# Kernel optimization log

Hardware: AMD Instinct MI355X
Metric: run time of the kernel (lower is better)

The kernel has to match this reference:

```python
import jax, jax.numpy as jnp
import numpy as np

N = 100000   # nodes
E = 1600000  # directed edges (avg degree 16)
IN, HID, OUT = 32, 64, 32


def setup_inputs() -> dict:
    key = jax.random.key(0)
    k0, k1, k2, k3 = jax.random.split(key, 4)
    x = jax.random.normal(k0, (N, IN), dtype=jnp.float32)
    edge_index = jax.random.randint(k1, (2, E), 0, N, dtype=jnp.int32)
    W1 = jax.random.normal(k2, (IN, HID), dtype=jnp.float32) * (1.0 / np.sqrt(IN))
    b1 = jnp.zeros((HID,), dtype=jnp.float32)
    W2 = jax.random.normal(k3, (HID, OUT), dtype=jnp.float32) * (1.0 / np.sqrt(HID))
    b2 = jnp.zeros((OUT,), dtype=jnp.float32)
    return {"x": x, "edge_index": edge_index, "W1": W1, "b1": b1, "W2": W2, "b2": b2}


def gcn_conv(x, src, dst, W, b, n):
    # GCNConv: D^{-1/2} (A + I) D^{-1/2} X W + b, deg computed after self-loops
    h = x @ W                                   # [N, d_out]
    ones = jnp.ones_like(dst, dtype=h.dtype)
    deg = jax.ops.segment_sum(ones, dst, num_segments=n)   # >= 1 (self-loops)
    dinv = jax.lax.rsqrt(jnp.maximum(deg, 1.0))
    norm = dinv[src] * dinv[dst]                # [E + N]
    agg = jax.ops.segment_sum(norm[:, None] * h[src], dst, num_segments=n)
    return agg + b


def reference(x, edge_index, W1, b1, W2, b2):
    n = x.shape[0]
    loop = jnp.arange(n, dtype=edge_index.dtype)
    src = jnp.concatenate([edge_index[0], loop])  # add self-loops once
    dst = jnp.concatenate([edge_index[1], loop])
    h = jax.nn.relu(gcn_conv(x, src, dst, W1, b1, n))
    # dropout omitted (eval mode)
    out = gcn_conv(h, src, dst, W2, b2, n)
    return out
```

## Files before the change

### kernel.cpp

```cpp
#include <hip/hip_runtime.h>

#define IN_F  32
#define HID_F 64
#define OUT_F 32

#define BKT_SHIFT 8
#define BKT_NODES 256
#define NBLK      1024

__device__ inline unsigned short f2bf(float f) {
    unsigned u = __float_as_uint(f);
    return (unsigned short)((u + 0x7FFF + ((u >> 16) & 1)) >> 16);
}
__device__ inline float bflo(unsigned w) { return __uint_as_float(w << 16); }
__device__ inline float bfhi(unsigned w) { return __uint_as_float(w & 0xFFFF0000u); }

__global__ __launch_bounds__(256) void count_kernel(const int* __restrict__ dst,
                                                    int* __restrict__ cnt, int E, int nb)
{
    __shared__ int hist[1024];
    int tid = threadIdx.x;
    for (int i = tid; i < nb; i += 256) hist[i] = 0;
    __syncthreads();
    for (int e = blockIdx.x * 256 + tid; e < E; e += NBLK * 256)
        atomicAdd(&hist[dst[e] >> BKT_SHIFT], 1);
    __syncthreads();
    for (int i = tid; i < nb; i += 256) cnt[i * NBLK + blockIdx.x] = hist[i];
}

__global__ __launch_bounds__(NBLK) void bsum_kernel(const int* __restrict__ cnt,
                                                    int* __restrict__ bsum)
{
    __shared__ int s[NBLK];
    int tid = threadIdx.x, b = blockIdx.x;
    s[tid] = cnt[b * NBLK + tid];
    __syncthreads();
    for (int off = NBLK / 2; off > 0; off >>= 1) {
        if (tid < off) s[tid] += s[tid + off];
        __syncthreads();
    }
    if (tid == 0) bsum[b] = s[0];
}

__global__ __launch_bounds__(512) void bscan_kernel(int* __restrict__ bsum, int nb,
                                                    int* __restrict__ cellstart, int nc,
                                                    int* __restrict__ rowstart, int n, int E)
{
    __shared__ int s[512];
    int tid = threadIdx.x;
    int my = (tid < nb) ? bsum[tid] : 0;
    s[tid] = my;
    __syncthreads();
    for (int off = 1; off < 512; off <<= 1) {
        int t = (tid >= off) ? s[tid - off] : 0;
        __syncthreads();
        s[tid] += t;
        __syncthreads();
    }
    if (tid < nb) bsum[tid] = s[tid] - my;
    if (tid == 0) { cellstart[nc] = E; rowstart[n] = E; }
}

__global__ __launch_bounds__(NBLK) void cscan_kernel(const int* __restrict__ cnt,
                                                     const int* __restrict__ bsum,
                                                     int* __restrict__ cellstart)
{
    __shared__ int s[NBLK];
    int tid = threadIdx.x, b = blockIdx.x;
    int my = cnt[b * NBLK + tid];
    s[tid] = my;
    __syncthreads();
    for (int off = 1; off < NBLK; off <<= 1) {
        int t = (tid >= off) ? s[tid - off] : 0;
        __syncthreads();
        s[tid] += t;
        __syncthreads();
    }
    cellstart[b * NBLK + tid] = bsum[b] + s[tid] - my;
}

__global__ __launch_bounds__(256) void append_kernel(
    const int* __restrict__ src, const int* __restrict__ dst,
    const int* __restrict__ cellstart, unsigned* __restrict__ pairs, int E, int nb)
{
    __shared__ int cur[1024];
    int tid = threadIdx.x;
    for (int i = tid; i < nb; i += 256) cur[i] = cellstart[i * NBLK + blockIdx.x];
    __syncthreads();
    for (int e = blockIdx.x * 256 + tid; e < E; e += NBLK * 256) {
        int d = dst[e];
        int pos = atomicAdd(&cur[d >> BKT_SHIFT], 1);
        pairs[pos] = ((unsigned)src[e] << BKT_SHIFT) | (unsigned)(d & (BKT_NODES - 1));
    }
}

__global__ __launch_bounds__(256) void place_kernel(
    const int* __restrict__ cellstart, const unsigned* __restrict__ pairs,
    const float* __restrict__ x,
    int* __restrict__ srcs, int* __restrict__ rowstart, float* __restrict__ dinv,
    unsigned* __restrict__ xs2, int n)
{
    __shared__ int hist[BKT_NODES];
    __shared__ int ofs[BKT_NODES];
    __shared__ float sdinv[BKT_NODES];
    int b = blockIdx.x, tid = threadIdx.x;
    int beg = cellstart[b * NBLK], end = cellstart[(b + 1) * NBLK];
    hist[tid] = 0;
    __syncthreads();
    for (int e = beg + tid; e < end; e += 256)
        atomicAdd(&hist[pairs[e] & (BKT_NODES - 1)], 1);
    __syncthreads();
    int my = hist[tid];
    ofs[tid] = my;
    __syncthreads();
    for (int off = 1; off < 256; off <<= 1) {
        int t = (tid >= off) ? ofs[tid - off] : 0;
        __syncthreads();
        ofs[tid] += t;
        __syncthreads();
    }
    int excl = ofs[tid] - my;
    int node = b * BKT_NODES + tid;
    float dv = rsqrtf((float)(my + 1));
    sdinv[tid] = dv;
    if (node < n) {
        rowstart[node] = beg + excl;
        dinv[node] = dv;
    }
    __syncthreads();
    ofs[tid] = excl;
    __syncthreads();
    for (int e = beg + tid; e < end; e += 256) {
        unsigned p = pairs[e];
        int dl = p & (BKT_NODES - 1);
        int pos = beg + atomicAdd(&ofs[dl], 1);
        srcs[pos] = (int)(p >> BKT_SHIFT);
    }
    const float4* x4 = (const float4*)x;
    uint2* xo = (uint2*)xs2;
    for (int idx = tid; idx < BKT_NODES * 8; idx += 256) {
        int nloc = idx >> 3, g = idx & 7;
        int nd = b * BKT_NODES + nloc;
        if (nd < n) {
            float d = sdinv[nloc];
            float4 v = x4[((size_t)nd << 3) + g];
            unsigned lo = (unsigned)f2bf(v.x * d) | ((unsigned)f2bf(v.y * d) << 16);
            unsigned hi = (unsigned)f2bf(v.z * d) | ((unsigned)f2bf(v.w * d) << 16);
            xo[((size_t)nd << 3) + g] = make_uint2(lo, hi);
        }
    }
}

__global__ __launch_bounds__(256) void fused1_kernel(
    const int* __restrict__ rowstart, const int* __restrict__ srcs,
    const unsigned* __restrict__ xs2, const float* __restrict__ dinv,
    const float* __restrict__ b1, const float* __restrict__ W1,
    const float* __restrict__ W2, unsigned* __restrict__ hs2p, int n)
{
    __shared__ float W1s[IN_F * HID_F];
    __shared__ float W2s[HID_F * OUT_F];
    __shared__ float grow[16][IN_F + 1];
    __shared__ float hrow[16][HID_F + 1];
    int tid = threadIdx.x;
    for (int t = tid; t < IN_F * HID_F; t += 256) W1s[t] = W1[t];
    for (int t = tid; t < HID_F * OUT_F; t += 256) W2s[t] = W2[t];

    int nl = tid >> 4;
    unsigned q = tid & 15;
    int node = blockIdx.x * 16 + nl;
    bool active = node < n;
    int nodec = active ? node : 0;

    int beg = rowstart[nodec], end = active ? rowstart[nodec + 1] : beg;
    unsigned ws = active ? xs2[((unsigned)nodec << 4) + q] : 0u;
    float a0l = bflo(ws), a0h = bfhi(ws);
    float a1l = 0.f, a1h = 0.f, a2l = 0.f, a2h = 0.f, a3l = 0.f, a3h = 0.f;
    float a4l = 0.f, a4h = 0.f, a5l = 0.f, a5h = 0.f, a6l = 0.f, a6h = 0.f;
    float a7l = 0.f, a7h = 0.f;
    int e = beg;
    for (; e + 8 <= end; e += 8) {
        unsigned o0 = ((unsigned)srcs[e]     << 4) + q, o1 = ((unsigned)srcs[e + 1] << 4) + q;
        unsigned o2 = ((unsigned)srcs[e + 2] << 4) + q, o3 = ((unsigned)srcs[e + 3] << 4) + q;
        unsigned o4 = ((unsigned)srcs[e + 4] << 4) + q, o5 = ((unsigned)srcs[e + 5] << 4) + q;
        unsigned o6 = ((unsigned)srcs[e + 6] << 4) + q, o7 = ((unsigned)srcs[e + 7] << 4) + q;
        unsigned w0 = xs2[o0], w1 = xs2[o1], w2 = xs2[o2], w3 = xs2[o3];
        unsigned w4 = xs2[o4], w5 = xs2[o5], w6 = xs2[o6], w7 = xs2[o7];
        a0l += bflo(w0); a0h += bfhi(w0); a1l += bflo(w1); a1h += bfhi(w1);
        a2l += bflo(w2); a2h += bfhi(w2); a3l += bflo(w3); a3h += bfhi(w3);
        a4l += bflo(w4); a4h += bfhi(w4); a5l += bflo(w5); a5h += bfhi(w5);
        a6l += bflo(w6); a6h += bfhi(w6); a7l += bflo(w7); a7h += bfhi(w7);
    }
    for (; e + 4 <= end; e += 4) {
        unsigned o0 = ((unsigned)srcs[e]     << 4) + q, o1 = ((unsigned)srcs[e + 1] << 4) + q;
        unsigned o2 = ((unsigned)srcs[e + 2] << 4) + q, o3 = ((unsigned)srcs[e + 3] << 4) + q;
        unsigned w0 = xs2[o0], w1 = xs2[o1], w2 = xs2[o2], w3 = xs2[o3];
        a0l += bflo(w0); a0h += bfhi(w0); a1l += bflo(w1); a1h += bfhi(w1);
        a2l += bflo(w2); a2h += bfhi(w2); a3l += bflo(w3); a3h += bfhi(w3);
    }
    for (; e < end; ++e) {
        unsigned w0 = xs2[((unsigned)srcs[e] << 4) + q];
        a0l += bflo(w0); a0h += bfhi(w0);
    }
    float dv = dinv[nodec];
    grow[nl][2 * q]     = dv * (((a0l + a1l) + (a2l + a3l)) + ((a4l + a5l) + (a6l + a7l)));
    grow[nl][2 * q + 1] = dv * (((a0h + a1h) + (a2h + a3h)) + ((a4h + a5h) + (a6h + a7h)));
    __syncthreads();

    float h0 = b1[q], h1 = b1[q + 16], h2 = b1[q + 32], h3 = b1[q + 48];
    #pragma unroll
    for (int k = 0; k < IN_F; ++k) {
        float gk = grow[nl][k];
        h0 += gk * W1s[k * HID_F + q];
        h1 += gk * W1s[k * HID_F + q + 16];
        h2 += gk * W1s[k * HID_F + q + 32];
        h3 += gk * W1s[k * HID_F + q + 48];
    }
    hrow[nl][q]      = fmaxf(h0, 0.f);
    hrow[nl][q + 16] = fmaxf(h1, 0.f);
    hrow[nl][q + 32] = fmaxf(h2, 0.f);
    hrow[nl][q + 48] = fmaxf(h3, 0.f);
    __syncthreads();

    float p0 = 0.f, p1 = 0.f;
    #pragma unroll
    for (int k = 0; k < HID_F; ++k) {
        float hk = hrow[nl][k];
        p0 += hk * W2s[k * OUT_F + 2 * q];
        p1 += hk * W2s[k * OUT_F + 2 * q + 1];
    }
    if (active) {
        unsigned pack = (unsigned)f2bf(dv * p0) | ((unsigned)f2bf(dv * p1) << 16);
        hs2p[((unsigned)node << 4) + q] = pack;
    }
}

__global__ __launch_bounds__(256) void agg2_kernel(
    const int* __restrict__ rowstart, const int* __restrict__ srcs,
    const unsigned* __restrict__ hs2p, const float* __restrict__ dinv,
    const float* __restrict__ b2, float* __restrict__ out, int n)
{
    int t = blockIdx.x * blockDim.x + threadIdx.x;
    int node = t >> 4;
    if (node >= n) return;
    unsigned q = t & 15;
    int beg = rowstart[node], end = rowstart[node + 1];
    unsigned ws = hs2p[((unsigned)node << 4) + q];
    float a0l = bflo(ws), a0h = bfhi(ws);
    float a1l = 0.f, a1h = 0.f, a2l = 0.f, a2h = 0.f, a3l = 0.f, a3h = 0.f;
    float a4l = 0.f, a4h = 0.f, a5l = 0.f, a5h = 0.f, a6l = 0.f, a6h = 0.f;
    float a7l = 0.f, a7h = 0.f;
    int e = beg;
    for (; e + 8 <= end; e += 8) {
        unsigned o0 = ((unsigned)srcs[e]     << 4) + q, o1 = ((unsigned)srcs[e + 1] << 4) + q;
        unsigned o2 = ((unsigned)srcs[e + 2] << 4) + q, o3 = ((unsigned)srcs[e + 3] << 4) + q;
        unsigned o4 = ((unsigned)srcs[e + 4] << 4) + q, o5 = ((unsigned)srcs[e + 5] << 4) + q;
        unsigned o6 = ((unsigned)srcs[e + 6] << 4) + q, o7 = ((unsigned)srcs[e + 7] << 4) + q;
        unsigned w0 = hs2p[o0], w1 = hs2p[o1], w2 = hs2p[o2], w3 = hs2p[o3];
        unsigned w4 = hs2p[o4], w5 = hs2p[o5], w6 = hs2p[o6], w7 = hs2p[o7];
        a0l += bflo(w0); a0h += bfhi(w0); a1l += bflo(w1); a1h += bfhi(w1);
        a2l += bflo(w2); a2h += bfhi(w2); a3l += bflo(w3); a3h += bfhi(w3);
        a4l += bflo(w4); a4h += bfhi(w4); a5l += bflo(w5); a5h += bfhi(w5);
        a6l += bflo(w6); a6h += bfhi(w6); a7l += bflo(w7); a7h += bfhi(w7);
    }
    for (; e + 4 <= end; e += 4) {
        unsigned o0 = ((unsigned)srcs[e]     << 4) + q, o1 = ((unsigned)srcs[e + 1] << 4) + q;
        unsigned o2 = ((unsigned)srcs[e + 2] << 4) + q, o3 = ((unsigned)srcs[e + 3] << 4) + q;
        unsigned w0 = hs2p[o0], w1 = hs2p[o1], w2 = hs2p[o2], w3 = hs2p[o3];
        a0l += bflo(w0); a0h += bfhi(w0); a1l += bflo(w1); a1h += bfhi(w1);
        a2l += bflo(w2); a2h += bfhi(w2); a3l += bflo(w3); a3h += bfhi(w3);
    }
    for (; e < end; ++e) {
        unsigned w0 = hs2p[((unsigned)srcs[e] << 4) + q];
        a0l += bflo(w0); a0h += bfhi(w0);
    }
    float dvv = dinv[node];
    float2 r;
    r.x = dvv * (((a0l + a1l) + (a2l + a3l)) + ((a4l + a5l) + (a6l + a7l))) + b2[2 * q];
    r.y = dvv * (((a0h + a1h) + (a2h + a3h)) + ((a4h + a5h) + (a6h + a7h))) + b2[2 * q + 1];
    ((float2*)out)[((size_t)node << 4) + q] = r;
}

extern "C" void kernel_launch(void* const* d_in, const int* in_sizes, int n_in,
                              void* d_out, int out_size, void* d_ws, size_t ws_size,
                              hipStream_t stream) {
    const float* x  = (const float*)d_in[0];
    const int*   ei = (const int*)  d_in[1];
    const float* W1 = (const float*)d_in[2];
    const float* b1 = (const float*)d_in[3];
    const float* W2 = (const float*)d_in[4];
    const float* b2 = (const float*)d_in[5];
    float* out = (float*)d_out;

    const int n = in_sizes[0] / IN_F;
    const int E = in_sizes[1] / 2;
    const int* src = ei;
    const int* dst = ei + E;

    const int nb = (n + BKT_NODES - 1) >> BKT_SHIFT;
    const int nc = nb * NBLK;

    int* ip = (int*)d_ws;
    int* cnt       = ip;                 ip += nc;
    int* cellstart = ip;                 ip += nc + 1;
    int* bsum      = ip;                 ip += nb + 1;
    int* rowstart  = ip;                 ip += n + 1;
    unsigned* pairs = (unsigned*)ip;     ip += E;
    int* srcs_srt  = ip;                 ip += E;
    float* dinv = (float*)ip;            ip += n;
    unsigned* xs2  = (unsigned*)ip;      ip += (size_t)n * IN_F / 2;
    unsigned* hs2p = (unsigned*)ip;

    count_kernel<<<NBLK, 256, 0, stream>>>(dst, cnt, E, nb);
    bsum_kernel <<<nb, NBLK, 0, stream>>>(cnt, bsum);
    bscan_kernel<<<1, 512, 0, stream>>>(bsum, nb, cellstart, nc, rowstart, n, E);
    cscan_kernel<<<nb, NBLK, 0, stream>>>(cnt, bsum, cellstart);
    append_kernel<<<NBLK, 256, 0, stream>>>(src, dst, cellstart, pairs, E, nb);
    place_kernel<<<nb, 256, 0, stream>>>(cellstart, pairs, x, srcs_srt, rowstart, dinv, xs2, n);

    fused1_kernel<<<(n + 15) / 16, 256, 0, stream>>>(rowstart, srcs_srt, xs2, dinv, b1, W1, W2, hs2p, n);
    agg2_kernel<<<((size_t)n * 16 + 255) / 256, 256, 0, stream>>>(rowstart, srcs_srt, hs2p, dinv, b2, out, n);
}
```

Baseline: 219.0 us.

## Process nodes in degree-sorted order to balance wavefront work in aggregation kernels

Adds a degree histogram in the placement kernel, a scan over degree bins, and a permutation fill. The fused layer-1 and layer-2 aggregation kernels then visit nodes grouped by in-degree, so the 16-lane groups in a wavefront run loops of similar length. The aim is to cut divergence and idle lanes caused by uneven neighbour counts. In exchange it adds two small kernels, a memset, global atomics, an extra indirection per node, and scattered output writes. It also halves NBLK, which changes the bucket-sort grid size.

```diff
diff --git a/kernel.cpp b/kernel.cpp
--- a/kernel.cpp
+++ b/kernel.cpp
@@ -6,7 +6,8 @@
 
 #define BKT_SHIFT 8
 #define BKT_NODES 256
-#define NBLK      1024
+#define NBLK      512
+#define DBINS     64
 
 __device__ inline unsigned short f2bf(float f) {
     unsigned u = __float_as_uint(f);
@@ -98,7 +99,7 @@
     const int* __restrict__ cellstart, const unsigned* __restrict__ pairs,
     const float* __restrict__ x,
     int* __restrict__ srcs, int* __restrict__ rowstart, float* __restrict__ dinv,
-    unsigned* __restrict__ xs2, int n)
+    unsigned* __restrict__ xs2, int* __restrict__ deghist, int n)
 {
     __shared__ int hist[BKT_NODES];
     __shared__ int ofs[BKT_NODES];
@@ -126,6 +127,7 @@
     if (node < n) {
         rowstart[node] = beg + excl;
         dinv[node] = dv;
+        atomicAdd(&deghist[min(my, DBINS - 1)], 1);
     }
     __syncthreads();
     ofs[tid] = excl;
@@ -151,7 +153,36 @@
     }
 }
 
+__global__ __launch_bounds__(DBINS) void binscan_kernel(const int* __restrict__ deghist,
+                                                        int* __restrict__ bincur)
+{
+    __shared__ int s[DBINS];
+    int tid = threadIdx.x;
+    int my = deghist[tid];
+    s[tid] = my;
+    __syncthreads();
+    for (int off = 1; off < DBINS; off <<= 1) {
+        int t = (tid >= off) ? s[tid - off] : 0;
+        __syncthreads();
+        s[tid] += t;
+        __syncthreads();
+    }
+    bincur[tid] = s[tid] - my;
+}
+
+__global__ void permfill_kernel(const int* __restrict__ rowstart, int* __restrict__ bincur,
+                                int* __restrict__ perm, int n)
+{
+    int node = blockIdx.x * blockDim.x + threadIdx.x;
+    if (node < n) {
+        int deg = rowstart[node + 1] - rowstart[node];
+        int pos = atomicAdd(&bincur[min(deg, DBINS - 1)], 1);
+        perm[pos] = node;
+    }
+}
+
 __global__ __launch_bounds__(256) void fused1_kernel(
+    const int* __restrict__ perm,
     const int* __restrict__ rowstart, const int* __restrict__ srcs,
     const unsigned* __restrict__ xs2, const float* __restrict__ dinv,
     const float* __restrict__ b1, const float* __restrict__ W1,
@@ -167,12 +198,12 @@
 
     int nl = tid >> 4;
     unsigned q = tid & 15;
-    int node = blockIdx.x * 16 + nl;
-    bool active = node < n;
-    int nodec = active ? node : 0;
-
-    int beg = rowstart[nodec], end = active ? rowstart[nodec + 1] : beg;
-    unsigned ws = active ? xs2[((unsigned)nodec << 4) + q] : 0u;
+    int g = blockIdx.x * 16 + nl;
+    bool active = g < n;
+    int node = active ? perm[g] : 0;
+
+    int beg = rowstart[node], end = active ? rowstart[node + 1] : beg;
+    unsigned ws = active ? xs2[((unsigned)node << 4) + q] : 0u;
     float a0l = bflo(ws), a0h = bfhi(ws);
     float a1l = 0.f, a1h = 0.f, a2l = 0.f, a2h = 0.f, a3l = 0.f, a3h = 0.f;
     float a4l = 0.f, a4h = 0.f, a5l = 0.f, a5h = 0.f, a6l = 0.f, a6h = 0.f;
@@ -201,7 +232,7 @@
         unsigned w0 = xs2[((unsigned)srcs[e] << 4) + q];
         a0l += bflo(w0); a0h += bfhi(w0);
     }
-    float dv = dinv[nodec];
+    float dv = dinv[node];
     grow[nl][2 * q]     = dv * (((a0l + a1l) + (a2l + a3l)) + ((a4l + a5l) + (a6l + a7l)));
     grow[nl][2 * q + 1] = dv * (((a0h + a1h) + (a2h + a3h)) + ((a4h + a5h) + (a6h + a7h)));
     __syncthreads();
@@ -235,13 +266,15 @@
 }
 
 __global__ __launch_bounds__(256) void agg2_kernel(
+    const int* __restrict__ perm,
     const int* __restrict__ rowstart, const int* __restrict__ srcs,
     const unsigned* __restrict__ hs2p, const float* __restrict__ dinv,
     const float* __restrict__ b2, float* __restrict__ out, int n)
 {
     int t = blockIdx.x * blockDim.x + threadIdx.x;
-    int node = t >> 4;
-    if (node >= n) return;
+    int g = t >> 4;
+    if (g >= n) return;
+    int node = perm[g];
     unsigned q = t & 15;
     int beg = rowstart[node], end = rowstart[node + 1];
     unsigned ws = hs2p[((unsigned)node << 4) + q];
@@ -304,19 +337,26 @@
     int* cellstart = ip;                 ip += nc + 1;
     int* bsum      = ip;                 ip += nb + 1;
     int* rowstart  = ip;                 ip += n + 1;
+    int* deghist   = ip;                 ip += DBINS;
+    int* bincur    = ip;                 ip += DBINS;
+    int* perm      = ip;                 ip += n;
     unsigned* pairs = (unsigned*)ip;     ip += E;
     int* srcs_srt  = ip;                 ip += E;
     float* dinv = (float*)ip;            ip += n;
     unsigned* xs2  = (unsigned*)ip;      ip += (size_t)n * IN_F / 2;
     unsigned* hs2p = (unsigned*)ip;
 
+    hipMemsetAsync(deghist, 0, DBINS * sizeof(int), stream);
+
     count_kernel<<<NBLK, 256, 0, stream>>>(dst, cnt, E, nb);
     bsum_kernel <<<nb, NBLK, 0, stream>>>(cnt, bsum);
     bscan_kernel<<<1, 512, 0, stream>>>(bsum, nb, cellstart, nc, rowstart, n, E);
     cscan_kernel<<<nb, NBLK, 0, stream>>>(cnt, bsum, cellstart);
     append_kernel<<<NBLK, 256, 0, stream>>>(src, dst, cellstart, pairs, E, nb);
-    place_kernel<<<nb, 256, 0, stream>>>(cellstart, pairs, x, srcs_srt, rowstart, dinv, xs2, n);
-
-    fused1_kernel<<<(n + 15) / 16, 256, 0, stream>>>(rowstart, srcs_srt, xs2, dinv, b1, W1, W2, hs2p, n);
-    agg2_kernel<<<((size_t)n * 16 + 255) / 256, 256, 0, stream>>>(rowstart, srcs_srt, hs2p, dinv, b2, out, n);
-}
+    place_kernel<<<nb, 256, 0, stream>>>(cellstart, pairs, x, srcs_srt, rowstart, dinv, xs2, deghist, n);
+    binscan_kernel<<<1, DBINS, 0, stream>>>(deghist, bincur);
+    permfill_kernel<<<(n + 255) / 256, 256, 0, stream>>>(rowstart, bincur, perm, n);
+
+    fused1_kernel<<<(n + 15) / 16, 256, 0, stream>>>(perm, rowstart, srcs_srt, xs2, dinv, b1, W1, W2, hs2p, n);
+    agg2_kernel<<<((size_t)n * 16 + 255) / 256, 256, 0, stream>>>(perm, rowstart, srcs_srt, hs2p, dinv, b2, out, n);
+}
```

After: 786.8 us. +259.3%, slower.
